# Kernel tuning notes

Hardware: AMD Instinct MI355X
Metric: run time of the kernel (lower is better)

## Reference

```python
import jax, jax.numpy as jnp
import numpy as np

B, N = 16, 48
NODE, EDGE, HID, MSG, LAYERS, TGT = 32, 16, 64, 64, 3, 128
NL = 128  # hidden width of cfg.net_layers / cfg.layers MLPs


def _lin(key, i, o):
    k1, k2 = jax.random.split(key)
    return (jax.random.normal(k1, (i, o), jnp.float32) * 0.05,
            jax.random.normal(k2, (o,), jnp.float32) * 0.05)


def setup_inputs() -> dict:
    key = jax.random.key(0)
    ks = jax.random.split(key, 16)
    g = (jax.random.uniform(ks[0], (B, N, N)) < 0.5).astype(jnp.float32)
    h0 = jax.random.normal(ks[1], (B, N, NODE), jnp.float32)
    e = jax.random.normal(ks[2], (B, N, N, EDGE), jnp.float32)
    msg_w0, msg_b0 = _lin(ks[3], EDGE, NL)
    msg_w1, msg_b1 = _lin(ks[4], NL, NL)
    msg_w2, msg_b2 = _lin(ks[5], NL, MSG * HID)
    gru_wih = jax.random.normal(ks[6], (3 * HID, MSG), jnp.float32) * 0.05
    gru_whh = jax.random.normal(ks[7], (3 * HID, HID), jnp.float32) * 0.05
    gru_bih = jax.random.normal(ks[8], (3 * HID,), jnp.float32) * 0.05
    gru_bhh = jax.random.normal(ks[9], (3 * HID,), jnp.float32) * 0.05
    r0_w0, r0_b0 = _lin(ks[10], 2 * HID, NL)
    r0_w1, r0_b1 = _lin(ks[11], NL, NL)
    r0_w2, r0_b2 = _lin(ks[12], NL, TGT)
    r1_w0, r1_b0 = _lin(ks[13], HID, NL)
    r1_w1, r1_b1 = _lin(ks[14], NL, NL)
    r1_w2, r1_b2 = _lin(ks[15], NL, TGT)
    return dict(g=g, h0=h0, e=e,
                msg_w0=msg_w0, msg_b0=msg_b0, msg_w1=msg_w1, msg_b1=msg_b1,
                msg_w2=msg_w2, msg_b2=msg_b2,
                gru_wih=gru_wih, gru_whh=gru_whh, gru_bih=gru_bih, gru_bhh=gru_bhh,
                r0_w0=r0_w0, r0_b0=r0_b0, r0_w1=r0_w1, r0_b1=r0_b1, r0_w2=r0_w2, r0_b2=r0_b2,
                r1_w0=r1_w0, r1_b0=r1_b0, r1_w1=r1_w1, r1_b1=r1_b1, r1_w2=r1_w2, r1_b2=r1_b2)


def _net(x, w0, b0, w1, b1, w2, b2):
    # Net: relu hidden layers, linear output (matches torch Net with 2 hidden layers)
    x = jax.nn.relu(x @ w0 + b0)
    x = jax.nn.relu(x @ w1 + b1)
    return x @ w2 + b2


def _gru_step(x, h, wih, whh, bih, bhh):
    # torch.nn.GRU single step; gate order r, z, n
    gi = x @ wih.T + bih
    gh = h @ whh.T + bhh
    r = jax.nn.sigmoid(gi[:, :HID] + gh[:, :HID])
    z = jax.nn.sigmoid(gi[:, HID:2 * HID] + gh[:, HID:2 * HID])
    n = jnp.tanh(gi[:, 2 * HID:] + r * gh[:, 2 * HID:])
    return (1.0 - z) * n + z * h


def reference(g, h0, e,
              msg_w0, msg_b0, msg_w1, msg_b1, msg_w2, msg_b2,
              gru_wih, gru_whh, gru_bih, gru_bhh,
              r0_w0, r0_b0, r0_w1, r0_b1, r0_w2, r0_b2,
              r1_w0, r1_b0, r1_w1, r1_b1, r1_w2, r1_b2):
    # pad h0 up to hidden size
    h_first = jnp.concatenate(
        [h0, jnp.zeros((B, N, HID - NODE), h0.dtype)], axis=2)
    node_mask = (jnp.sum(h0, axis=2) > 0).astype(h0.dtype)[..., None]  # [B,N,1]

    # per-edge weight matrices from edge features (same every layer in the
    # original torch code, so compute once): [B*N*N, MSG, HID]
    m_w = _net(e.reshape(-1, EDGE), msg_w0, msg_b0, msg_w1, msg_b1,
               msg_w2, msg_b2).reshape(-1, MSG, HID)

    h_t = h_first
    for _ in range(LAYERS):
        h_feat = h_t.reshape(-1, HID)  # [B*N, HID]
        # faithful to torch: expand on last dim then view(-1, HID),
        # which interleaves the hidden and neighbor axes in memory order
        h_w_rows = jnp.broadcast_to(
            h_feat[:, :, None], (B * N, HID, N)).reshape(-1, HID)
        msg = jnp.einsum('emh,eh->em', m_w, h_w_rows)  # [B*N*N, MSG]
        msg = msg.reshape(B, N, N, MSG)
        agg = jnp.sum(g[..., None] * msg, axis=1)  # masked sum over dim 1 -> [B,N,MSG]
        h_new = _gru_step(agg.reshape(-1, MSG), h_t.reshape(-1, HID),
                          gru_wih, gru_whh, gru_bih, gru_bhh).reshape(B, N, HID)
        h_t = node_mask * h_new

    # readout: Net0(cat[h_0, h_T]) * Net1(h_T), masked by h_0 activity, summed over nodes
    gate_in = jnp.concatenate([h_first, h_t], axis=-1)  # [B,N,2*HID]
    nn_res = (_net(gate_in, r0_w0, r0_b0, r0_w1, r0_b1, r0_w2, r0_b2) *
              _net(h_t, r1_w0, r1_b0, r1_w1, r1_b1, r1_w2, r1_b2))  # [B,N,TGT]
    read_mask = (jnp.sum(h_first, axis=2) > 0).astype(nn_res.dtype)[..., None]
    res = jnp.sum(read_mask * nn_res, axis=1)  # [B,TGT]
    return jax.nn.sigmoid(res)
```

## Files before the change

kernel.cpp:

```cpp
#include <hip/hip_runtime.h>
#include <cmath>

#define B_ 16
#define N_ 48
#define HID_ 64
#define NL_ 128
#define NNODE_ (B_*N_)
#define NEDGE_ (B_*N_*N_)

__device__ __forceinline__ float sigmoidf_(float x){ return 1.0f/(1.0f+expf(-x)); }

__global__ void k_prep(const float* __restrict__ w2, const float* __restrict__ b2,
                       const float* __restrict__ h0,
                       const float* __restrict__ wih, const float* __restrict__ whh,
                       const float* __restrict__ w1,
                       float* __restrict__ A, float* __restrict__ Bm,
                       float* __restrict__ Ab, float* __restrict__ Bb,
                       float* __restrict__ hfirst, float* __restrict__ mask,
                       float* __restrict__ wihT, float* __restrict__ whhT,
                       float* __restrict__ w1T)
{
    int idx = blockIdx.x*256 + threadIdx.x;
    if (idx < 24576) {
        int r = idx >> 13;
        int c = (idx >> 6) & 127;
        int m = idx & 63;
        int t = 48 - 16*r;
        const float* src = w2 + c*4096 + m*64;
        float a = 0.f, b = 0.f;
        for (int k = 0; k < 64; k++){ float v = src[k]; if (k < t) a += v; else b += v; }
        A[idx] = a; Bm[idx] = b;
    } else if (idx < 24768) {
        int i2 = idx - 24576;
        int r = i2 >> 6, m = i2 & 63;
        int t = 48 - 16*r;
        const float* src = b2 + m*64;
        float a = 0.f, b = 0.f;
        for (int k = 0; k < 64; k++){ float v = src[k]; if (k < t) a += v; else b += v; }
        Ab[i2] = a; Bb[i2] = b;
    } else if (idx < 73920) {
        int i3 = idx - 24768;
        int node = i3 >> 6, m = i3 & 63;
        hfirst[i3] = (m < 32) ? h0[node*32 + m] : 0.f;
        if (m == 0) {
            float s = 0.f;
            for (int k = 0; k < 32; k++) s += h0[node*32 + k];
            mask[node] = (s > 0.f) ? 1.f : 0.f;
        }
    } else if (idx < 98496) {
        int i4 = idx - 73920;
        if (i4 < 12288) {
            int k = i4 / 192, col = i4 - k*192;
            wihT[i4] = wih[col*64 + k];
        } else {
            int i5 = i4 - 12288;
            int k = i5 / 192, col = i5 - k*192;
            whhT[i5] = whh[col*64 + k];
        }
    } else if (idx < 114880) {
        int i6 = idx - 98496;
        int o = i6 >> 7, i = i6 & 127;
        w1T[i6] = w1[i*128 + o];
    }
}

__global__ __launch_bounds__(256) void k_mlp(
    const float* __restrict__ ein, const float* __restrict__ w0, const float* __restrict__ b0,
    const float* __restrict__ w1T, const float* __restrict__ b1,
    float* __restrict__ relu2)
{
    __shared__ __align__(16) float x1s[64*132];
    int tid = threadIdx.x;
    int et = tid & 15, ot = tid >> 4;
    int o0 = ot * 8;
    size_t e0 = (size_t)blockIdx.x * 64;

    float acc[4][8];
    {
        float4 ba = *(const float4*)&b0[o0];
        float4 bb = *(const float4*)&b0[o0 + 4];
        #pragma unroll
        for (int q = 0; q < 4; q++){
            acc[q][0]=ba.x; acc[q][1]=ba.y; acc[q][2]=ba.z; acc[q][3]=ba.w;
            acc[q][4]=bb.x; acc[q][5]=bb.y; acc[q][6]=bb.z; acc[q][7]=bb.w;
        }
    }
    #pragma unroll
    for (int i4 = 0; i4 < 4; i4++){
        float4 ev[4];
        #pragma unroll
        for (int q = 0; q < 4; q++)
            ev[q] = *(const float4*)&ein[(e0 + q*16 + et)*16 + i4*4];
        #pragma unroll
        for (int d = 0; d < 4; d++){
            int i = i4*4 + d;
            float4 wa = *(const float4*)&w0[i*128 + o0];
            float4 wb = *(const float4*)&w0[i*128 + o0 + 4];
            #pragma unroll
            for (int q = 0; q < 4; q++){
                float xi = (d==0) ? ev[q].x : (d==1) ? ev[q].y : (d==2) ? ev[q].z : ev[q].w;
                acc[q][0] += xi*wa.x; acc[q][1] += xi*wa.y;
                acc[q][2] += xi*wa.z; acc[q][3] += xi*wa.w;
                acc[q][4] += xi*wb.x; acc[q][5] += xi*wb.y;
                acc[q][6] += xi*wb.z; acc[q][7] += xi*wb.w;
            }
        }
    }
    #pragma unroll
    for (int q = 0; q < 4; q++){
        int e = q*16 + et;
        float4 s0 = make_float4(fmaxf(acc[q][0],0.f), fmaxf(acc[q][1],0.f),
                                fmaxf(acc[q][2],0.f), fmaxf(acc[q][3],0.f));
        float4 s1 = make_float4(fmaxf(acc[q][4],0.f), fmaxf(acc[q][5],0.f),
                                fmaxf(acc[q][6],0.f), fmaxf(acc[q][7],0.f));
        *(float4*)&x1s[e*132 + o0]     = s0;
        *(float4*)&x1s[e*132 + o0 + 4] = s1;
    }
    __syncthreads();

    float a2[4][8];
    {
        float4 ba = *(const float4*)&b1[o0];
        float4 bb = *(const float4*)&b1[o0 + 4];
        #pragma unroll
        for (int q = 0; q < 4; q++){
            a2[q][0]=ba.x; a2[q][1]=ba.y; a2[q][2]=ba.z; a2[q][3]=ba.w;
            a2[q][4]=bb.x; a2[q][5]=bb.y; a2[q][6]=bb.z; a2[q][7]=bb.w;
        }
    }
    for (int i4 = 0; i4 < 32; i4++){
        int i = i4*4;
        float4 wv[8];
        #pragma unroll
        for (int r2 = 0; r2 < 8; r2++)
            wv[r2] = *(const float4*)&w1T[(size_t)(o0 + r2)*128 + i];
        #pragma unroll
        for (int q = 0; q < 4; q++){
            float4 xv = *(const float4*)&x1s[(q*16 + et)*132 + i];
            #pragma unroll
            for (int r2 = 0; r2 < 8; r2++){
                a2[q][r2] += xv.x*wv[r2].x + xv.y*wv[r2].y
                           + xv.z*wv[r2].z + xv.w*wv[r2].w;
            }
        }
    }
    #pragma unroll
    for (int q = 0; q < 4; q++){
        size_t e = e0 + q*16 + et;
        float4 s0 = make_float4(fmaxf(a2[q][0],0.f), fmaxf(a2[q][1],0.f),
                                fmaxf(a2[q][2],0.f), fmaxf(a2[q][3],0.f));
        float4 s1 = make_float4(fmaxf(a2[q][4],0.f), fmaxf(a2[q][5],0.f),
                                fmaxf(a2[q][6],0.f), fmaxf(a2[q][7],0.f));
        *(float4*)&relu2[e*128 + o0]     = s0;
        *(float4*)&relu2[e*128 + o0 + 4] = s1;
    }
}

__global__ __launch_bounds__(256) void k_layer(
    const float* __restrict__ hin, float* __restrict__ hout,
    const float* __restrict__ relu2,
    const float* __restrict__ A, const float* __restrict__ Bm,
    const float* __restrict__ Ab, const float* __restrict__ Bb,
    const float* __restrict__ g, const float* __restrict__ mask,
    const float* __restrict__ wihT, const float* __restrict__ whhT,
    const float* __restrict__ bih, const float* __restrict__ bhh)
{
    int bj = blockIdx.x;
    int b = bj / 48, j = bj - b*48;
    int r = j % 3;
    int p0 = j + j/3;
    int tid = threadIdx.x;
    int base = b*48;
    __shared__ float hs[64], wAs[48], wBs[48];
    __shared__ float pU[2][128], pV[2][128];
    __shared__ float Us[128], Vs[128];
    __shared__ float pC[4][64];
    __shared__ float sAB[2];
    __shared__ float aggs[64], gi[192], gh[192];

    if (tid < 64) hs[tid] = hin[(size_t)bj*64 + tid];
    else if (tid < 112){
        int i = tid - 64;
        int node = base + i;
        float gv = g[(size_t)node*48 + j];
        wAs[i] = gv * hin[(size_t)node*64 + p0];
        wBs[i] = gv * hin[(size_t)node*64 + p0 + 1];
    }
    __syncthreads();
    if (tid < 2){
        const float* src = tid ? wBs : wAs;
        float s = 0.f;
        for (int i = 0; i < 48; i++) s += src[i];
        sAB[tid] = s;
    }
    {
        int c = tid & 127, half = tid >> 7;
        const float* r2b = relu2 + ((size_t)base*48 + j)*128 + c;
        float aU = 0.f, aV = 0.f;
        for (int ii = 0; ii < 24; ii++){
            int i = half*24 + ii;
            float v = r2b[(size_t)i*6144];
            aU += wAs[i]*v; aV += wBs[i]*v;
        }
        pU[half][c] = aU; pV[half][c] = aV;
    }
    __syncthreads();
    if (tid < 128){ Us[tid] = pU[0][tid] + pU[1][tid]; Vs[tid] = pV[0][tid] + pV[1][tid]; }
    __syncthreads();
    {
        int m = tid & 63, cg = tid >> 6;
        const float* Arp = A  + r*8192 + m;
        const float* Brp = Bm + r*8192 + m;
        float a = 0.f;
        for (int cc = 0; cc < 32; cc++){
            int c = cg*32 + cc;
            a += Us[c]*Arp[c*64] + Vs[c]*Brp[c*64];
        }
        pC[cg][m] = a;
    }
    __syncthreads();
    if (tid < 64){
        aggs[tid] = pC[0][tid] + pC[1][tid] + pC[2][tid] + pC[3][tid]
                  + sAB[0]*Ab[r*64 + tid] + sAB[1]*Bb[r*64 + tid];
    }
    __syncthreads();
    if (tid < 192){
        float gacc = bih[tid], hacc = bhh[tid];
        for (int k = 0; k < 64; k++){
            gacc += aggs[k] * wihT[k*192 + tid];
            hacc += hs[k]   * whhT[k*192 + tid];
        }
        gi[tid] = gacc; gh[tid] = hacc;
    }
    __syncthreads();
    if (tid < 64){
        float rr = sigmoidf_(gi[tid] + gh[tid]);
        float zz = sigmoidf_(gi[64+tid] + gh[64+tid]);
        float nn = tanhf(gi[128+tid] + rr*gh[128+tid]);
        float hnew = (1.f - zz)*nn + zz*hs[tid];
        hout[(size_t)bj*64 + tid] = mask[bj] * hnew;
    }
}

__device__ __forceinline__ void rd_layer(
    const float* __restrict__ Xs, const float* __restrict__ W,
    const float* __restrict__ bias, float* __restrict__ Ys,
    int dim, int o, int ng, bool do_relu)
{
    float a0 = bias[o];
    float a1 = a0;
    for (int i = 0; i < dim; i += 4){
        float w0 = W[(size_t)(i+0)*128 + o];
        float w1 = W[(size_t)(i+1)*128 + o];
        float w2 = W[(size_t)(i+2)*128 + o];
        float w3 = W[(size_t)(i+3)*128 + o];
        const float4 x0 = *(const float4*)&Xs[ng*128 + i];
        const float4 x1 = *(const float4*)&Xs[(ng+2)*128 + i];
        a0 += x0.x*w0 + x0.y*w1 + x0.z*w2 + x0.w*w3;
        a1 += x1.x*w0 + x1.y*w1 + x1.z*w2 + x1.w*w3;
    }
    if (do_relu){ a0 = fmaxf(a0, 0.f); a1 = fmaxf(a1, 0.f); }
    Ys[ng*128 + o] = a0;
    Ys[(ng+2)*128 + o] = a1;
}

__global__ __launch_bounds__(256) void k_read(
    const float* __restrict__ hfirst, const float* __restrict__ hT,
    const float* __restrict__ mask,
    const float* __restrict__ w00, const float* __restrict__ b00,
    const float* __restrict__ w01, const float* __restrict__ b01,
    const float* __restrict__ w02, const float* __restrict__ b02,
    const float* __restrict__ w10, const float* __restrict__ b10,
    const float* __restrict__ w11, const float* __restrict__ b11,
    const float* __restrict__ w12, const float* __restrict__ b12,
    float* __restrict__ partial)
{
    __shared__ __align__(16) float xs[4*128];
    __shared__ __align__(16) float ys[4*128];
    __shared__ __align__(16) float zs[4*128];
    __shared__ __align__(16) float os0[4*128];
    __shared__ float mS[4];
    int tid = threadIdx.x;
    int b = blockIdx.x / 12, gg = blockIdx.x - b*12;
    int node0 = b*48 + gg*4;
    int o = tid & 127, ng = tid >> 7;
    if (tid < 4) mS[tid] = mask[node0 + tid];
    for (int i = tid; i < 4*128; i += 256){
        int r = i >> 7, c = i & 127;
        xs[i] = (c < 64) ? hfirst[(size_t)(node0+r)*64 + c]
                         : hT[(size_t)(node0+r)*64 + (c - 64)];
    }
    __syncthreads();
    rd_layer(xs,      w00, b00, ys,  128, o, ng, true);  __syncthreads();
    rd_layer(ys,      w01, b01, zs,  128, o, ng, true);  __syncthreads();
    rd_layer(zs,      w02, b02, os0, 128, o, ng, false); __syncthreads();
    rd_layer(xs + 64, w10, b10, ys,  64,  o, ng, true);  __syncthreads();
    rd_layer(ys,      w11, b11, zs,  128, o, ng, true);  __syncthreads();
    {
        float a0 = b12[o];
        float a1 = a0;
        for (int i = 0; i < 128; i += 4){
            float w0 = w12[(size_t)(i+0)*128 + o];
            float w1 = w12[(size_t)(i+1)*128 + o];
            float w2 = w12[(size_t)(i+2)*128 + o];
            float w3 = w12[(size_t)(i+3)*128 + o];
            const float4 x0 = *(const float4*)&zs[ng*128 + i];
            const float4 x1 = *(const float4*)&zs[(ng+2)*128 + i];
            a0 += x0.x*w0 + x0.y*w1 + x0.z*w2 + x0.w*w3;
            a1 += x1.x*w0 + x1.y*w1 + x1.z*w2 + x1.w*w3;
        }
        float s = mS[ng]   * os0[ng*128 + o]     * a0
                + mS[ng+2] * os0[(ng+2)*128 + o] * a1;
        __syncthreads();
        ys[ng*128 + o] = s;
    }
    __syncthreads();
    if (tid < 128)
        partial[(size_t)blockIdx.x*128 + tid] = ys[tid] + ys[128 + tid];
}

__global__ void k_final(const float* __restrict__ partial, float* __restrict__ out)
{
    int idx = blockIdx.x*256 + threadIdx.x;
    if (idx < B_*128){
        int b = idx >> 7, t = idx & 127;
        float s = 0.f;
        for (int c = 0; c < 12; c++) s += partial[(size_t)(b*12 + c)*128 + t];
        out[idx] = 1.0f / (1.0f + expf(-s));
    }
}

extern "C" void kernel_launch(void* const* d_in, const int* in_sizes, int n_in,
                              void* d_out, int out_size, void* d_ws, size_t ws_size,
                              hipStream_t stream)
{
    (void)in_sizes; (void)n_in; (void)out_size; (void)ws_size;
    const float* g    = (const float*)d_in[0];
    const float* h0   = (const float*)d_in[1];
    const float* e    = (const float*)d_in[2];
    const float* mw0  = (const float*)d_in[3];
    const float* mb0  = (const float*)d_in[4];
    const float* mw1  = (const float*)d_in[5];
    const float* mb1  = (const float*)d_in[6];
    const float* mw2  = (const float*)d_in[7];
    const float* mb2  = (const float*)d_in[8];
    const float* wih  = (const float*)d_in[9];
    const float* whh  = (const float*)d_in[10];
    const float* bih  = (const float*)d_in[11];
    const float* bhh  = (const float*)d_in[12];
    const float* r0w0 = (const float*)d_in[13];
    const float* r0b0 = (const float*)d_in[14];
    const float* r0w1 = (const float*)d_in[15];
    const float* r0b1 = (const float*)d_in[16];
    const float* r0w2 = (const float*)d_in[17];
    const float* r0b2 = (const float*)d_in[18];
    const float* r1w0 = (const float*)d_in[19];
    const float* r1b0 = (const float*)d_in[20];
    const float* r1w1 = (const float*)d_in[21];
    const float* r1b1 = (const float*)d_in[22];
    const float* r1w2 = (const float*)d_in[23];
    const float* r1b2 = (const float*)d_in[24];
    float* out = (float*)d_out;

    float* ws     = (float*)d_ws;
    float* A      = ws;
    float* Bm     = A      + 24576;
    float* Ab     = Bm     + 24576;
    float* Bb     = Ab     + 192;
    float* hfirst = Bb     + 192;
    float* hA     = hfirst + 49152;
    float* hB     = hA     + 49152;
    float* mask   = hB     + 49152;
    float* wihT   = mask   + 768;
    float* whhT   = wihT   + 12288;
    float* w1T    = whhT   + 12288;
    float* part   = w1T    + 16384;
    float* relu2  = part   + 24576;

    k_prep<<<449, 256, 0, stream>>>(mw2, mb2, h0, wih, whh, mw1,
                                    A, Bm, Ab, Bb, hfirst, mask, wihT, whhT, w1T);
    k_mlp<<<576, 256, 0, stream>>>(e, mw0, mb0, w1T, mb1, relu2);
    k_layer<<<768, 256, 0, stream>>>(hfirst, hA, relu2, A, Bm, Ab, Bb, g, mask,
                                     wihT, whhT, bih, bhh);
    k_layer<<<768, 256, 0, stream>>>(hA, hB, relu2, A, Bm, Ab, Bb, g, mask,
                                     wihT, whhT, bih, bhh);
    k_layer<<<768, 256, 0, stream>>>(hB, hA, relu2, A, Bm, Ab, Bb, g, mask,
                                     wihT, whhT, bih, bhh);
    k_read<<<192, 256, 0, stream>>>(hfirst, hA, mask,
                                    r0w0, r0b0, r0w1, r0b1, r0w2, r0b2,
                                    r1w0, r1b0, r1w1, r1b1, r1w2, r1b2, part);
    k_final<<<8, 256, 0, stream>>>(part, out);
}
```

Before: 192.8 us.

## Fuse edge MLP with first GRU layer and last layer with readout

Result: slower. 228.4 us (+18.5%).

```diff
diff --git a/kernel.cpp b/kernel.cpp
--- a/kernel.cpp
+++ b/kernel.cpp
@@ -3,22 +3,16 @@
 
 #define B_ 16
 #define N_ 48
-#define HID_ 64
-#define NL_ 128
-#define NNODE_ (B_*N_)
-#define NEDGE_ (B_*N_*N_)
 
 __device__ __forceinline__ float sigmoidf_(float x){ return 1.0f/(1.0f+expf(-x)); }
 
 __global__ void k_prep(const float* __restrict__ w2, const float* __restrict__ b2,
                        const float* __restrict__ h0,
                        const float* __restrict__ wih, const float* __restrict__ whh,
-                       const float* __restrict__ w1,
                        float* __restrict__ A, float* __restrict__ Bm,
                        float* __restrict__ Ab, float* __restrict__ Bb,
                        float* __restrict__ hfirst, float* __restrict__ mask,
-                       float* __restrict__ wihT, float* __restrict__ whhT,
-                       float* __restrict__ w1T)
+                       float* __restrict__ wihT, float* __restrict__ whhT)
 {
     int idx = blockIdx.x*256 + threadIdx.x;
     if (idx < 24576) {
@@ -57,47 +51,58 @@
             int k = i5 / 192, col = i5 - k*192;
             whhT[i5] = whh[col*64 + k];
         }
-    } else if (idx < 114880) {
-        int i6 = idx - 98496;
-        int o = i6 >> 7, i = i6 & 127;
-        w1T[i6] = w1[i*128 + o];
     }
 }
 
-__global__ __launch_bounds__(256) void k_mlp(
+__global__ __launch_bounds__(256, 3) void k1_mlp_l0(
     const float* __restrict__ ein, const float* __restrict__ w0, const float* __restrict__ b0,
-    const float* __restrict__ w1T, const float* __restrict__ b1,
-    float* __restrict__ relu2)
+    const float* __restrict__ w1, const float* __restrict__ b1,
+    const float* __restrict__ g, const float* __restrict__ h0,
+    const float* __restrict__ mask,
+    const float* __restrict__ A, const float* __restrict__ Bm,
+    const float* __restrict__ Ab, const float* __restrict__ Bb,
+    const float* __restrict__ wihT, const float* __restrict__ whhT,
+    const float* __restrict__ bih, const float* __restrict__ bhh,
+    float* __restrict__ relu2, float* __restrict__ hout)
 {
-    __shared__ __align__(16) float x1s[64*132];
-    int tid = threadIdx.x;
-    int et = tid & 15, ot = tid >> 4;
-    int o0 = ot * 8;
-    size_t e0 = (size_t)blockIdx.x * 64;
-
-    float acc[4][8];
+    __shared__ __align__(16) float smem[12480];
+    float* x1s = smem;
+    float* r2s = smem + 6336;
+    const int tid  = threadIdx.x;
+    const int bj   = blockIdx.x;
+    const int b    = bj / 48, j = bj - b*48;
+    const int base = b*48;
+
+    const int et = tid & 15;
+    const int o0 = (tid >> 4) * 8;
+    size_t eg[3];
+    #pragma unroll
+    for (int q = 0; q < 3; q++)
+        eg[q] = ((size_t)(base + q*16 + et)*48 + j);
+
+    float acc[3][8];
     {
         float4 ba = *(const float4*)&b0[o0];
         float4 bb = *(const float4*)&b0[o0 + 4];
         #pragma unroll
-        for (int q = 0; q < 4; q++){
+        for (int q = 0; q < 3; q++){
             acc[q][0]=ba.x; acc[q][1]=ba.y; acc[q][2]=ba.z; acc[q][3]=ba.w;
             acc[q][4]=bb.x; acc[q][5]=bb.y; acc[q][6]=bb.z; acc[q][7]=bb.w;
         }
     }
     #pragma unroll
     for (int i4 = 0; i4 < 4; i4++){
-        float4 ev[4];
+        float4 ev[3];
         #pragma unroll
-        for (int q = 0; q < 4; q++)
-            ev[q] = *(const float4*)&ein[(e0 + q*16 + et)*16 + i4*4];
+        for (int q = 0; q < 3; q++)
+            ev[q] = *(const float4*)&ein[eg[q]*16 + i4*4];
         #pragma unroll
         for (int d = 0; d < 4; d++){
             int i = i4*4 + d;
             float4 wa = *(const float4*)&w0[i*128 + o0];
             float4 wb = *(const float4*)&w0[i*128 + o0 + 4];
             #pragma unroll
-            for (int q = 0; q < 4; q++){
+            for (int q = 0; q < 3; q++){
                 float xi = (d==0) ? ev[q].x : (d==1) ? ev[q].y : (d==2) ? ev[q].z : ev[q].w;
                 acc[q][0] += xi*wa.x; acc[q][1] += xi*wa.y;
                 acc[q][2] += xi*wa.z; acc[q][3] += xi*wa.w;
@@ -107,52 +112,148 @@
         }
     }
     #pragma unroll
-    for (int q = 0; q < 4; q++){
-        int e = q*16 + et;
-        float4 s0 = make_float4(fmaxf(acc[q][0],0.f), fmaxf(acc[q][1],0.f),
-                                fmaxf(acc[q][2],0.f), fmaxf(acc[q][3],0.f));
-        float4 s1 = make_float4(fmaxf(acc[q][4],0.f), fmaxf(acc[q][5],0.f),
-                                fmaxf(acc[q][6],0.f), fmaxf(acc[q][7],0.f));
-        *(float4*)&x1s[e*132 + o0]     = s0;
-        *(float4*)&x1s[e*132 + o0 + 4] = s1;
-    }
-    __syncthreads();
-
-    float a2[4][8];
+    for (int q = 0; q < 3; q++){
+        int el = q*16 + et;
+        *(float4*)&x1s[el*132 + o0] =
+            make_float4(fmaxf(acc[q][0],0.f), fmaxf(acc[q][1],0.f),
+                        fmaxf(acc[q][2],0.f), fmaxf(acc[q][3],0.f));
+        *(float4*)&x1s[el*132 + o0 + 4] =
+            make_float4(fmaxf(acc[q][4],0.f), fmaxf(acc[q][5],0.f),
+                        fmaxf(acc[q][6],0.f), fmaxf(acc[q][7],0.f));
+    }
+    __syncthreads();
+
+    float a2[3][8];
     {
         float4 ba = *(const float4*)&b1[o0];
         float4 bb = *(const float4*)&b1[o0 + 4];
         #pragma unroll
-        for (int q = 0; q < 4; q++){
+        for (int q = 0; q < 3; q++){
             a2[q][0]=ba.x; a2[q][1]=ba.y; a2[q][2]=ba.z; a2[q][3]=ba.w;
             a2[q][4]=bb.x; a2[q][5]=bb.y; a2[q][6]=bb.z; a2[q][7]=bb.w;
         }
     }
     for (int i4 = 0; i4 < 32; i4++){
         int i = i4*4;
-        float4 wv[8];
+        float4 w0a = *(const float4*)&w1[(size_t)(i+0)*128 + o0];
+        float4 w0b = *(const float4*)&w1[(size_t)(i+0)*128 + o0 + 4];
+        float4 w1a = *(const float4*)&w1[(size_t)(i+1)*128 + o0];
+        float4 w1b = *(const float4*)&w1[(size_t)(i+1)*128 + o0 + 4];
+        float4 w2a = *(const float4*)&w1[(size_t)(i+2)*128 + o0];
+        float4 w2b = *(const float4*)&w1[(size_t)(i+2)*128 + o0 + 4];
+        float4 w3a = *(const float4*)&w1[(size_t)(i+3)*128 + o0];
+        float4 w3b = *(const float4*)&w1[(size_t)(i+3)*128 + o0 + 4];
+        float4 xv[3];
         #pragma unroll
-        for (int r2 = 0; r2 < 8; r2++)
-            wv[r2] = *(const float4*)&w1T[(size_t)(o0 + r2)*128 + i];
+        for (int q = 0; q < 3; q++)
+            xv[q] = *(const float4*)&x1s[(q*16 + et)*132 + i];
         #pragma unroll
-        for (int q = 0; q < 4; q++){
-            float4 xv = *(const float4*)&x1s[(q*16 + et)*132 + i];
-            #pragma unroll
-            for (int r2 = 0; r2 < 8; r2++){
-                a2[q][r2] += xv.x*wv[r2].x + xv.y*wv[r2].y
-                           + xv.z*wv[r2].z + xv.w*wv[r2].w;
-            }
+        for (int q = 0; q < 3; q++){
+            float4 x = xv[q];
+            a2[q][0] += x.x*w0a.x + x.y*w1a.x + x.z*w2a.x + x.w*w3a.x;
+            a2[q][1] += x.x*w0a.y + x.y*w1a.y + x.z*w2a.y + x.w*w3a.y;
+            a2[q][2] += x.x*w0a.z + x.y*w1a.z + x.z*w2a.z + x.w*w3a.z;
+            a2[q][3] += x.x*w0a.w + x.y*w1a.w + x.z*w2a.w + x.w*w3a.w;
+            a2[q][4] += x.x*w0b.x + x.y*w1b.x + x.z*w2b.x + x.w*w3b.x;
+            a2[q][5] += x.x*w0b.y + x.y*w1b.y + x.z*w2b.y + x.w*w3b.y;
+            a2[q][6] += x.x*w0b.z + x.y*w1b.z + x.z*w2b.z + x.w*w3b.z;
+            a2[q][7] += x.x*w0b.w + x.y*w1b.w + x.z*w2b.w + x.w*w3b.w;
         }
     }
     #pragma unroll
-    for (int q = 0; q < 4; q++){
-        size_t e = e0 + q*16 + et;
+    for (int q = 0; q < 3; q++){
+        int el = q*16 + et;
         float4 s0 = make_float4(fmaxf(a2[q][0],0.f), fmaxf(a2[q][1],0.f),
                                 fmaxf(a2[q][2],0.f), fmaxf(a2[q][3],0.f));
         float4 s1 = make_float4(fmaxf(a2[q][4],0.f), fmaxf(a2[q][5],0.f),
                                 fmaxf(a2[q][6],0.f), fmaxf(a2[q][7],0.f));
-        *(float4*)&relu2[e*128 + o0]     = s0;
-        *(float4*)&relu2[e*128 + o0 + 4] = s1;
+        *(float4*)&r2s[el*128 + o0]     = s0;
+        *(float4*)&r2s[el*128 + o0 + 4] = s1;
+        *(float4*)&relu2[eg[q]*128 + o0]     = s0;
+        *(float4*)&relu2[eg[q]*128 + o0 + 4] = s1;
+    }
+    __syncthreads();
+
+    float* hs   = smem;
+    float* wAs  = smem + 64;
+    float* wBs  = smem + 112;
+    float* sAB  = smem + 160;
+    float* pU   = smem + 162;
+    float* pV   = smem + 418;
+    float* Us   = smem + 674;
+    float* Vs   = smem + 802;
+    float* pC   = smem + 930;
+    float* aggs = smem + 1186;
+    float* gi   = smem + 1250;
+    float* gh   = smem + 1442;
+
+    const int r  = j % 3;
+    const int q0 = j + j/3;
+
+    if (tid < 64) hs[tid] = (tid < 32) ? h0[bj*32 + tid] : 0.f;
+    else if (tid < 112){
+        int i = tid - 64;
+        int node = base + i;
+        float gv = g[(size_t)node*48 + j];
+        float ha = (q0   < 32) ? h0[node*32 + q0]     : 0.f;
+        float hb = (q0+1 < 32) ? h0[node*32 + q0 + 1] : 0.f;
+        wAs[i] = gv * ha;
+        wBs[i] = gv * hb;
+    }
+    __syncthreads();
+    if (tid < 2){
+        const float* src = tid ? wBs : wAs;
+        float s = 0.f;
+        for (int i = 0; i < 48; i++) s += src[i];
+        sAB[tid] = s;
+    }
+    {
+        int c = tid & 127, half = tid >> 7;
+        const float* rb = r2s + c;
+        float aU = 0.f, aV = 0.f;
+        for (int ii = 0; ii < 24; ii++){
+            int i = half*24 + ii;
+            float v = rb[i*128];
+            aU += wAs[i]*v; aV += wBs[i]*v;
+        }
+        pU[half*128 + c] = aU; pV[half*128 + c] = aV;
+    }
+    __syncthreads();
+    if (tid < 128){ Us[tid] = pU[tid] + pU[128 + tid]; }
+    else { int c = tid - 128; Vs[c] = pV[c] + pV[128 + c]; }
+    __syncthreads();
+    {
+        int m = tid & 63, cg2 = tid >> 6;
+        const float* Arp = A  + r*8192 + m;
+        const float* Brp = Bm + r*8192 + m;
+        float a = 0.f;
+        for (int cc = 0; cc < 32; cc++){
+            int c = cg2*32 + cc;
+            a += Us[c]*Arp[c*64] + Vs[c]*Brp[c*64];
+        }
+        pC[cg2*64 + m] = a;
+    }
+    __syncthreads();
+    if (tid < 64){
+        aggs[tid] = pC[tid] + pC[64+tid] + pC[128+tid] + pC[192+tid]
+                  + sAB[0]*Ab[r*64 + tid] + sAB[1]*Bb[r*64 + tid];
+    }
+    __syncthreads();
+    if (tid < 192){
+        float gacc = bih[tid], hacc = bhh[tid];
+        for (int k = 0; k < 64; k++){
+            gacc += aggs[k] * wihT[k*192 + tid];
+            hacc += hs[k]   * whhT[k*192 + tid];
+        }
+        gi[tid] = gacc; gh[tid] = hacc;
+    }
+    __syncthreads();
+    if (tid < 64){
+        float rr = sigmoidf_(gi[tid] + gh[tid]);
+        float zz = sigmoidf_(gi[64+tid] + gh[64+tid]);
+        float nn = tanhf(gi[128+tid] + rr*gh[128+tid]);
+        float hnew = (1.f - zz)*nn + zz*hs[tid];
+        hout[(size_t)bj*64 + tid] = mask[bj] * hnew;
     }
 }
 
@@ -242,90 +343,173 @@
     }
 }
 
-__device__ __forceinline__ void rd_layer(
-    const float* __restrict__ Xs, const float* __restrict__ W,
-    const float* __restrict__ bias, float* __restrict__ Ys,
-    int dim, int o, int ng, bool do_relu)
-{
-    float a0 = bias[o];
-    float a1 = a0;
-    for (int i = 0; i < dim; i += 4){
-        float w0 = W[(size_t)(i+0)*128 + o];
-        float w1 = W[(size_t)(i+1)*128 + o];
-        float w2 = W[(size_t)(i+2)*128 + o];
-        float w3 = W[(size_t)(i+3)*128 + o];
-        const float4 x0 = *(const float4*)&Xs[ng*128 + i];
-        const float4 x1 = *(const float4*)&Xs[(ng+2)*128 + i];
-        a0 += x0.x*w0 + x0.y*w1 + x0.z*w2 + x0.w*w3;
-        a1 += x1.x*w0 + x1.y*w1 + x1.z*w2 + x1.w*w3;
-    }
-    if (do_relu){ a0 = fmaxf(a0, 0.f); a1 = fmaxf(a1, 0.f); }
-    Ys[ng*128 + o] = a0;
-    Ys[(ng+2)*128 + o] = a1;
-}
-
-__global__ __launch_bounds__(256) void k_read(
-    const float* __restrict__ hfirst, const float* __restrict__ hT,
-    const float* __restrict__ mask,
+__global__ __launch_bounds__(256) void k3_layer_read(
+    const float* __restrict__ hin,
+    const float* __restrict__ relu2,
+    const float* __restrict__ A, const float* __restrict__ Bm,
+    const float* __restrict__ Ab, const float* __restrict__ Bb,
+    const float* __restrict__ g, const float* __restrict__ mask,
+    const float* __restrict__ wihT, const float* __restrict__ whhT,
+    const float* __restrict__ bih, const float* __restrict__ bhh,
+    const float* __restrict__ hfirst,
     const float* __restrict__ w00, const float* __restrict__ b00,
     const float* __restrict__ w01, const float* __restrict__ b01,
     const float* __restrict__ w02, const float* __restrict__ b02,
     const float* __restrict__ w10, const float* __restrict__ b10,
     const float* __restrict__ w11, const float* __restrict__ b11,
     const float* __restrict__ w12, const float* __restrict__ b12,
-    float* __restrict__ partial)
+    float* __restrict__ part)
 {
-    __shared__ __align__(16) float xs[4*128];
-    __shared__ __align__(16) float ys[4*128];
-    __shared__ __align__(16) float zs[4*128];
-    __shared__ __align__(16) float os0[4*128];
-    __shared__ float mS[4];
+    int bj = blockIdx.x;
+    int b = bj / 48, j = bj - b*48;
+    int r = j % 3;
+    int p0 = j + j/3;
     int tid = threadIdx.x;
-    int b = blockIdx.x / 12, gg = blockIdx.x - b*12;
-    int node0 = b*48 + gg*4;
-    int o = tid & 127, ng = tid >> 7;
-    if (tid < 4) mS[tid] = mask[node0 + tid];
-    for (int i = tid; i < 4*128; i += 256){
-        int r = i >> 7, c = i & 127;
-        xs[i] = (c < 64) ? hfirst[(size_t)(node0+r)*64 + c]
-                         : hT[(size_t)(node0+r)*64 + (c - 64)];
-    }
-    __syncthreads();
-    rd_layer(xs,      w00, b00, ys,  128, o, ng, true);  __syncthreads();
-    rd_layer(ys,      w01, b01, zs,  128, o, ng, true);  __syncthreads();
-    rd_layer(zs,      w02, b02, os0, 128, o, ng, false); __syncthreads();
-    rd_layer(xs + 64, w10, b10, ys,  64,  o, ng, true);  __syncthreads();
-    rd_layer(ys,      w11, b11, zs,  128, o, ng, true);  __syncthreads();
-    {
-        float a0 = b12[o];
-        float a1 = a0;
-        for (int i = 0; i < 128; i += 4){
-            float w0 = w12[(size_t)(i+0)*128 + o];
-            float w1 = w12[(size_t)(i+1)*128 + o];
-            float w2 = w12[(size_t)(i+2)*128 + o];
-            float w3 = w12[(size_t)(i+3)*128 + o];
-            const float4 x0 = *(const float4*)&zs[ng*128 + i];
-            const float4 x1 = *(const float4*)&zs[(ng+2)*128 + i];
-            a0 += x0.x*w0 + x0.y*w1 + x0.z*w2 + x0.w*w3;
-            a1 += x1.x*w0 + x1.y*w1 + x1.z*w2 + x1.w*w3;
-        }
-        float s = mS[ng]   * os0[ng*128 + o]     * a0
-                + mS[ng+2] * os0[(ng+2)*128 + o] * a1;
-        __syncthreads();
-        ys[ng*128 + o] = s;
-    }
-    __syncthreads();
-    if (tid < 128)
-        partial[(size_t)blockIdx.x*128 + tid] = ys[tid] + ys[128 + tid];
+    int base = b*48;
+    __shared__ float hs[64], wAs[48], wBs[48];
+    __shared__ float pU[2][128], pV[2][128];
+    __shared__ float Us[128], Vs[128];
+    __shared__ float pC[4][64];
+    __shared__ float sAB[2];
+    __shared__ float aggs[64], gi[192], gh[192];
+    __shared__ float hfs[64], hTs[64];
+    __shared__ float ps[256], bufA[128], bufB[128], os0[128];
+
+    if (tid < 64) hs[tid] = hin[(size_t)bj*64 + tid];
+    else if (tid < 112){
+        int i = tid - 64;
+        int node = base + i;
+        float gv = g[(size_t)node*48 + j];
+        wAs[i] = gv * hin[(size_t)node*64 + p0];
+        wBs[i] = gv * hin[(size_t)node*64 + p0 + 1];
+    }
+    else if (tid < 176){
+        hfs[tid - 112] = hfirst[(size_t)bj*64 + (tid - 112)];
+    }
+    __syncthreads();
+    if (tid < 2){
+        const float* src = tid ? wBs : wAs;
+        float s = 0.f;
+        for (int i = 0; i < 48; i++) s += src[i];
+        sAB[tid] = s;
+    }
+    {
+        int c = tid & 127, half = tid >> 7;
+        const float* r2b = relu2 + ((size_t)base*48 + j)*128 + c;
+        float aU = 0.f, aV = 0.f;
+        for (int ii = 0; ii < 24; ii++){
+            int i = half*24 + ii;
+            float v = r2b[(size_t)i*6144];
+            aU += wAs[i]*v; aV += wBs[i]*v;
+        }
+        pU[half][c] = aU; pV[half][c] = aV;
+    }
+    __syncthreads();
+    if (tid < 128){ Us[tid] = pU[0][tid] + pU[1][tid]; Vs[tid] = pV[0][tid] + pV[1][tid]; }
+    __syncthreads();
+    {
+        int m = tid & 63, cg = tid >> 6;
+        const float* Arp = A  + r*8192 + m;
+        const float* Brp = Bm + r*8192 + m;
+        float a = 0.f;
+        for (int cc = 0; cc < 32; cc++){
+            int c = cg*32 + cc;
+            a += Us[c]*Arp[c*64] + Vs[c]*Brp[c*64];
+        }
+        pC[cg][m] = a;
+    }
+    __syncthreads();
+    if (tid < 64){
+        aggs[tid] = pC[0][tid] + pC[1][tid] + pC[2][tid] + pC[3][tid]
+                  + sAB[0]*Ab[r*64 + tid] + sAB[1]*Bb[r*64 + tid];
+    }
+    __syncthreads();
+    if (tid < 192){
+        float gacc = bih[tid], hacc = bhh[tid];
+        for (int k = 0; k < 64; k++){
+            gacc += aggs[k] * wihT[k*192 + tid];
+            hacc += hs[k]   * whhT[k*192 + tid];
+        }
+        gi[tid] = gacc; gh[tid] = hacc;
+    }
+    __syncthreads();
+    if (tid < 64){
+        float rr = sigmoidf_(gi[tid] + gh[tid]);
+        float zz = sigmoidf_(gi[64+tid] + gh[64+tid]);
+        float nn = tanhf(gi[128+tid] + rr*gh[128+tid]);
+        float hnew = (1.f - zz)*nn + zz*hs[tid];
+        hTs[tid] = mask[bj] * hnew;
+    }
+    __syncthreads();
+
+    int o = tid & 127, hh = tid >> 7;
+    {
+        float a = 0.f;
+        for (int i = hh*64; i < hh*64 + 64; i++){
+            float x = (i < 64) ? hfs[i] : hTs[i - 64];
+            a += x * w00[(size_t)i*128 + o];
+        }
+        ps[hh*128 + o] = a;
+    }
+    __syncthreads();
+    if (tid < 128) bufA[o] = fmaxf(b00[o] + ps[o] + ps[128 + o], 0.f);
+    __syncthreads();
+    {
+        float a = 0.f;
+        for (int i = hh*64; i < hh*64 + 64; i++)
+            a += bufA[i] * w01[(size_t)i*128 + o];
+        ps[hh*128 + o] = a;
+    }
+    __syncthreads();
+    if (tid < 128) bufB[o] = fmaxf(b01[o] + ps[o] + ps[128 + o], 0.f);
+    __syncthreads();
+    {
+        float a = 0.f;
+        for (int i = hh*64; i < hh*64 + 64; i++)
+            a += bufB[i] * w02[(size_t)i*128 + o];
+        ps[hh*128 + o] = a;
+    }
+    __syncthreads();
+    if (tid < 128) os0[o] = b02[o] + ps[o] + ps[128 + o];
+    __syncthreads();
+    {
+        float a = 0.f;
+        for (int i = hh*32; i < hh*32 + 32; i++)
+            a += hTs[i] * w10[(size_t)i*128 + o];
+        ps[hh*128 + o] = a;
+    }
+    __syncthreads();
+    if (tid < 128) bufA[o] = fmaxf(b10[o] + ps[o] + ps[128 + o], 0.f);
+    __syncthreads();
+    {
+        float a = 0.f;
+        for (int i = hh*64; i < hh*64 + 64; i++)
+            a += bufA[i] * w11[(size_t)i*128 + o];
+        ps[hh*128 + o] = a;
+    }
+    __syncthreads();
+    if (tid < 128) bufB[o] = fmaxf(b11[o] + ps[o] + ps[128 + o], 0.f);
+    __syncthreads();
+    {
+        float a = 0.f;
+        for (int i = hh*64; i < hh*64 + 64; i++)
+            a += bufB[i] * w12[(size_t)i*128 + o];
+        ps[hh*128 + o] = a;
+    }
+    __syncthreads();
+    if (tid < 128){
+        float r1o = b12[o] + ps[o] + ps[128 + o];
+        part[(size_t)bj*128 + o] = mask[bj] * os0[o] * r1o;
+    }
 }
 
-__global__ void k_final(const float* __restrict__ partial, float* __restrict__ out)
+__global__ void k_final(const float* __restrict__ part, float* __restrict__ out)
 {
     int idx = blockIdx.x*256 + threadIdx.x;
     if (idx < B_*128){
         int b = idx >> 7, t = idx & 127;
         float s = 0.f;
-        for (int c = 0; c < 12; c++) s += partial[(size_t)(b*12 + c)*128 + t];
+        for (int n = 0; n < 48; n++) s += part[(size_t)(b*48 + n)*128 + t];
         out[idx] = 1.0f / (1.0f + expf(-s));
     }
 }
@@ -373,21 +557,20 @@
     float* mask   = hB     + 49152;
     float* wihT   = mask   + 768;
     float* whhT   = wihT   + 12288;
-    float* w1T    = whhT   + 12288;
-    float* part   = w1T    + 16384;
-    float* relu2  = part   + 24576;
-
-    k_prep<<<449, 256, 0, stream>>>(mw2, mb2, h0, wih, whh, mw1,
-                                    A, Bm, Ab, Bb, hfirst, mask, wihT, whhT, w1T);
-    k_mlp<<<576, 256, 0, stream>>>(e, mw0, mb0, w1T, mb1, relu2);
-    k_layer<<<768, 256, 0, stream>>>(hfirst, hA, relu2, A, Bm, Ab, Bb, g, mask,
-                                     wihT, whhT, bih, bhh);
+    float* part   = whhT   + 12288;
+    float* relu2  = part   + 98304;
+
+    k_prep<<<385, 256, 0, stream>>>(mw2, mb2, h0, wih, whh,
+                                    A, Bm, Ab, Bb, hfirst, mask, wihT, whhT);
+    k1_mlp_l0<<<768, 256, 0, stream>>>(e, mw0, mb0, mw1, mb1, g, h0, mask,
+                                       A, Bm, Ab, Bb, wihT, whhT, bih, bhh,
+                                       relu2, hA);
     k_layer<<<768, 256, 0, stream>>>(hA, hB, relu2, A, Bm, Ab, Bb, g, mask,
                                      wihT, whhT, bih, bhh);
-    k_layer<<<768, 256, 0, stream>>>(hB, hA, relu2, A, Bm, Ab, Bb, g, mask,
-                                     wihT, whhT, bih, bhh);
-    k_read<<<192, 256, 0, stream>>>(hfirst, hA, mask,
-                                    r0w0, r0b0, r0w1, r0b1, r0w2, r0b2,
-                                    r1w0, r1b0, r1w1, r1b1, r1w2, r1b2, part);
+    k3_layer_read<<<768, 256, 0, stream>>>(hB, relu2, A, Bm, Ab, Bb, g, mask,
+                                           wihT, whhT, bih, bhh, hfirst,
+                                           r0w0, r0b0, r0w1, r0b1, r0w2, r0b2,
+                                           r1w0, r1b0, r1w1, r1b1, r1w2, r1b2,
+                                           part);
     k_final<<<8, 256, 0, stream>>>(part, out);
 }
```

## Fuse edge MLP with first message-passing layer using destination-major edge layout

Applied to the files above, without the earlier changes.

After: 196.2 us. About the same (+1.7%).

```diff
diff --git a/kernel.cpp b/kernel.cpp
--- a/kernel.cpp
+++ b/kernel.cpp
@@ -3,22 +3,18 @@
 
 #define B_ 16
 #define N_ 48
-#define HID_ 64
-#define NL_ 128
-#define NNODE_ (B_*N_)
-#define NEDGE_ (B_*N_*N_)
 
 __device__ __forceinline__ float sigmoidf_(float x){ return 1.0f/(1.0f+expf(-x)); }
 
 __global__ void k_prep(const float* __restrict__ w2, const float* __restrict__ b2,
                        const float* __restrict__ h0,
                        const float* __restrict__ wih, const float* __restrict__ whh,
-                       const float* __restrict__ w1,
+                       const float* __restrict__ e,
                        float* __restrict__ A, float* __restrict__ Bm,
                        float* __restrict__ Ab, float* __restrict__ Bb,
                        float* __restrict__ hfirst, float* __restrict__ mask,
                        float* __restrict__ wihT, float* __restrict__ whhT,
-                       float* __restrict__ w1T)
+                       float* __restrict__ eT)
 {
     int idx = blockIdx.x*256 + threadIdx.x;
     if (idx < 24576) {
@@ -57,47 +53,65 @@
             int k = i5 / 192, col = i5 - k*192;
             whhT[i5] = whh[col*64 + k];
         }
-    } else if (idx < 114880) {
+    } else if (idx < 245952) {
         int i6 = idx - 98496;
-        int o = i6 >> 7, i = i6 & 127;
-        w1T[i6] = w1[i*128 + o];
-    }
-}
-
-__global__ __launch_bounds__(256) void k_mlp(
-    const float* __restrict__ ein, const float* __restrict__ w0, const float* __restrict__ b0,
-    const float* __restrict__ w1T, const float* __restrict__ b1,
-    float* __restrict__ relu2)
-{
-    __shared__ __align__(16) float x1s[64*132];
-    int tid = threadIdx.x;
-    int et = tid & 15, ot = tid >> 4;
-    int o0 = ot * 8;
-    size_t e0 = (size_t)blockIdx.x * 64;
-
-    float acc[4][8];
+        int d4 = i6 & 3;
+        int E  = i6 >> 2;
+        int j  = E % 48;
+        int bi = E / 48;
+        int i  = bi % 48;
+        int b  = bi / 48;
+        float4 v = *(const float4*)&e[(size_t)i6*4];
+        *(float4*)&eT[(((size_t)(b*48 + j)*48 + i)*4 + d4)*4] = v;
+    }
+}
+
+__global__ __launch_bounds__(256, 3) void k1_mlp_l0(
+    const float* __restrict__ eT, const float* __restrict__ w0, const float* __restrict__ b0,
+    const float* __restrict__ w1, const float* __restrict__ b1,
+    const float* __restrict__ g, const float* __restrict__ h0,
+    const float* __restrict__ mask,
+    const float* __restrict__ A, const float* __restrict__ Bm,
+    const float* __restrict__ Ab, const float* __restrict__ Bb,
+    const float* __restrict__ wihT, const float* __restrict__ whhT,
+    const float* __restrict__ bih, const float* __restrict__ bhh,
+    float* __restrict__ relu2T, float* __restrict__ hout)
+{
+    __shared__ __align__(16) float smem[12480];
+    float* x1s = smem;
+    float* r2s = smem + 6336;
+    const int tid  = threadIdx.x;
+    const int bj   = blockIdx.x;
+    const int b    = bj / 48, j = bj - b*48;
+    const int base = b*48;
+
+    const int et = tid & 15;
+    const int o0 = (tid >> 4) * 8;
+    const size_t ebase = (size_t)bj * 48;
+
+    float acc[3][8];
     {
         float4 ba = *(const float4*)&b0[o0];
         float4 bb = *(const float4*)&b0[o0 + 4];
         #pragma unroll
-        for (int q = 0; q < 4; q++){
+        for (int q = 0; q < 3; q++){
             acc[q][0]=ba.x; acc[q][1]=ba.y; acc[q][2]=ba.z; acc[q][3]=ba.w;
             acc[q][4]=bb.x; acc[q][5]=bb.y; acc[q][6]=bb.z; acc[q][7]=bb.w;
         }
     }
     #pragma unroll
     for (int i4 = 0; i4 < 4; i4++){
-        float4 ev[4];
+        float4 ev[3];
         #pragma unroll
-        for (int q = 0; q < 4; q++)
-            ev[q] = *(const float4*)&ein[(e0 + q*16 + et)*16 + i4*4];
+        for (int q = 0; q < 3; q++)
+            ev[q] = *(const float4*)&eT[(ebase + q*16 + et)*16 + i4*4];
         #pragma unroll
         for (int d = 0; d < 4; d++){
             int i = i4*4 + d;
             float4 wa = *(const float4*)&w0[i*128 + o0];
             float4 wb = *(const float4*)&w0[i*128 + o0 + 4];
             #pragma unroll
-            for (int q = 0; q < 4; q++){
+            for (int q = 0; q < 3; q++){
                 float xi = (d==0) ? ev[q].x : (d==1) ? ev[q].y : (d==2) ? ev[q].z : ev[q].w;
                 acc[q][0] += xi*wa.x; acc[q][1] += xi*wa.y;
                 acc[q][2] += xi*wa.z; acc[q][3] += xi*wa.w;
@@ -107,58 +121,154 @@
         }
     }
     #pragma unroll
-    for (int q = 0; q < 4; q++){
-        int e = q*16 + et;
-        float4 s0 = make_float4(fmaxf(acc[q][0],0.f), fmaxf(acc[q][1],0.f),
-                                fmaxf(acc[q][2],0.f), fmaxf(acc[q][3],0.f));
-        float4 s1 = make_float4(fmaxf(acc[q][4],0.f), fmaxf(acc[q][5],0.f),
-                                fmaxf(acc[q][6],0.f), fmaxf(acc[q][7],0.f));
-        *(float4*)&x1s[e*132 + o0]     = s0;
-        *(float4*)&x1s[e*132 + o0 + 4] = s1;
-    }
-    __syncthreads();
-
-    float a2[4][8];
+    for (int q = 0; q < 3; q++){
+        int el = q*16 + et;
+        *(float4*)&x1s[el*132 + o0] =
+            make_float4(fmaxf(acc[q][0],0.f), fmaxf(acc[q][1],0.f),
+                        fmaxf(acc[q][2],0.f), fmaxf(acc[q][3],0.f));
+        *(float4*)&x1s[el*132 + o0 + 4] =
+            make_float4(fmaxf(acc[q][4],0.f), fmaxf(acc[q][5],0.f),
+                        fmaxf(acc[q][6],0.f), fmaxf(acc[q][7],0.f));
+    }
+    __syncthreads();
+
+    float a2[3][8];
     {
         float4 ba = *(const float4*)&b1[o0];
         float4 bb = *(const float4*)&b1[o0 + 4];
         #pragma unroll
-        for (int q = 0; q < 4; q++){
+        for (int q = 0; q < 3; q++){
             a2[q][0]=ba.x; a2[q][1]=ba.y; a2[q][2]=ba.z; a2[q][3]=ba.w;
             a2[q][4]=bb.x; a2[q][5]=bb.y; a2[q][6]=bb.z; a2[q][7]=bb.w;
         }
     }
     for (int i4 = 0; i4 < 32; i4++){
         int i = i4*4;
-        float4 wv[8];
+        float4 w0a = *(const float4*)&w1[(size_t)(i+0)*128 + o0];
+        float4 w0b = *(const float4*)&w1[(size_t)(i+0)*128 + o0 + 4];
+        float4 w1a = *(const float4*)&w1[(size_t)(i+1)*128 + o0];
+        float4 w1b = *(const float4*)&w1[(size_t)(i+1)*128 + o0 + 4];
+        float4 w2a = *(const float4*)&w1[(size_t)(i+2)*128 + o0];
+        float4 w2b = *(const float4*)&w1[(size_t)(i+2)*128 + o0 + 4];
+        float4 w3a = *(const float4*)&w1[(size_t)(i+3)*128 + o0];
+        float4 w3b = *(const float4*)&w1[(size_t)(i+3)*128 + o0 + 4];
+        float4 xv[3];
         #pragma unroll
-        for (int r2 = 0; r2 < 8; r2++)
-            wv[r2] = *(const float4*)&w1T[(size_t)(o0 + r2)*128 + i];
+        for (int q = 0; q < 3; q++)
+            xv[q] = *(const float4*)&x1s[(q*16 + et)*132 + i];
         #pragma unroll
-        for (int q = 0; q < 4; q++){
-            float4 xv = *(const float4*)&x1s[(q*16 + et)*132 + i];
-            #pragma unroll
-            for (int r2 = 0; r2 < 8; r2++){
-                a2[q][r2] += xv.x*wv[r2].x + xv.y*wv[r2].y
-                           + xv.z*wv[r2].z + xv.w*wv[r2].w;
-            }
+        for (int q = 0; q < 3; q++){
+            float4 x = xv[q];
+            a2[q][0] += x.x*w0a.x + x.y*w1a.x + x.z*w2a.x + x.w*w3a.x;
+            a2[q][1] += x.x*w0a.y + x.y*w1a.y + x.z*w2a.y + x.w*w3a.y;
+            a2[q][2] += x.x*w0a.z + x.y*w1a.z + x.z*w2a.z + x.w*w3a.z;
+            a2[q][3] += x.x*w0a.w + x.y*w1a.w + x.z*w2a.w + x.w*w3a.w;
+            a2[q][4] += x.x*w0b.x + x.y*w1b.x + x.z*w2b.x + x.w*w3b.x;
+            a2[q][5] += x.x*w0b.y + x.y*w1b.y + x.z*w2b.y + x.w*w3b.y;
+            a2[q][6] += x.x*w0b.z + x.y*w1b.z + x.z*w2b.z + x.w*w3b.z;
+            a2[q][7] += x.x*w0b.w + x.y*w1b.w + x.z*w2b.w + x.w*w3b.w;
         }
     }
     #pragma unroll
-    for (int q = 0; q < 4; q++){
-        size_t e = e0 + q*16 + et;
+    for (int q = 0; q < 3; q++){
+        int el = q*16 + et;
         float4 s0 = make_float4(fmaxf(a2[q][0],0.f), fmaxf(a2[q][1],0.f),
                                 fmaxf(a2[q][2],0.f), fmaxf(a2[q][3],0.f));
         float4 s1 = make_float4(fmaxf(a2[q][4],0.f), fmaxf(a2[q][5],0.f),
                                 fmaxf(a2[q][6],0.f), fmaxf(a2[q][7],0.f));
-        *(float4*)&relu2[e*128 + o0]     = s0;
-        *(float4*)&relu2[e*128 + o0 + 4] = s1;
+        *(float4*)&r2s[el*128 + o0]     = s0;
+        *(float4*)&r2s[el*128 + o0 + 4] = s1;
+        *(float4*)&relu2T[(ebase + el)*128 + o0]     = s0;
+        *(float4*)&relu2T[(ebase + el)*128 + o0 + 4] = s1;
+    }
+    __syncthreads();
+
+    float* hs   = smem;
+    float* wAs  = smem + 64;
+    float* wBs  = smem + 112;
+    float* sAB  = smem + 160;
+    float* pU   = smem + 162;
+    float* pV   = smem + 418;
+    float* Us   = smem + 674;
+    float* Vs   = smem + 802;
+    float* pC   = smem + 930;
+    float* aggs = smem + 1186;
+    float* gi   = smem + 1250;
+    float* gh   = smem + 1442;
+
+    const int r  = j % 3;
+    const int q0 = j + j/3;
+
+    if (tid < 64) hs[tid] = (tid < 32) ? h0[bj*32 + tid] : 0.f;
+    else if (tid < 112){
+        int i = tid - 64;
+        int node = base + i;
+        float gv = g[(size_t)node*48 + j];
+        float ha = (q0   < 32) ? h0[node*32 + q0]     : 0.f;
+        float hb = (q0+1 < 32) ? h0[node*32 + q0 + 1] : 0.f;
+        wAs[i] = gv * ha;
+        wBs[i] = gv * hb;
+    }
+    __syncthreads();
+    if (tid < 2){
+        const float* src = tid ? wBs : wAs;
+        float s = 0.f;
+        for (int i = 0; i < 48; i++) s += src[i];
+        sAB[tid] = s;
+    }
+    {
+        int c = tid & 127, half = tid >> 7;
+        const float* rb = r2s + c;
+        float aU = 0.f, aV = 0.f;
+        for (int ii = 0; ii < 24; ii++){
+            int i = half*24 + ii;
+            float v = rb[i*128];
+            aU += wAs[i]*v; aV += wBs[i]*v;
+        }
+        pU[half*128 + c] = aU; pV[half*128 + c] = aV;
+    }
+    __syncthreads();
+    if (tid < 128){ Us[tid] = pU[tid] + pU[128 + tid]; }
+    else { int c = tid - 128; Vs[c] = pV[c] + pV[128 + c]; }
+    __syncthreads();
+    {
+        int m = tid & 63, cg2 = tid >> 6;
+        const float* Arp = A  + r*8192 + m;
+        const float* Brp = Bm + r*8192 + m;
+        float a = 0.f;
+        for (int cc = 0; cc < 32; cc++){
+            int c = cg2*32 + cc;
+            a += Us[c]*Arp[c*64] + Vs[c]*Brp[c*64];
+        }
+        pC[cg2*64 + m] = a;
+    }
+    __syncthreads();
+    if (tid < 64){
+        aggs[tid] = pC[tid] + pC[64+tid] + pC[128+tid] + pC[192+tid]
+                  + sAB[0]*Ab[r*64 + tid] + sAB[1]*Bb[r*64 + tid];
+    }
+    __syncthreads();
+    if (tid < 192){
+        float gacc = bih[tid], hacc = bhh[tid];
+        for (int k = 0; k < 64; k++){
+            gacc += aggs[k] * wihT[k*192 + tid];
+            hacc += hs[k]   * whhT[k*192 + tid];
+        }
+        gi[tid] = gacc; gh[tid] = hacc;
+    }
+    __syncthreads();
+    if (tid < 64){
+        float rr = sigmoidf_(gi[tid] + gh[tid]);
+        float zz = sigmoidf_(gi[64+tid] + gh[64+tid]);
+        float nn = tanhf(gi[128+tid] + rr*gh[128+tid]);
+        float hnew = (1.f - zz)*nn + zz*hs[tid];
+        hout[(size_t)bj*64 + tid] = mask[bj] * hnew;
     }
 }
 
 __global__ __launch_bounds__(256) void k_layer(
     const float* __restrict__ hin, float* __restrict__ hout,
-    const float* __restrict__ relu2,
+    const float* __restrict__ relu2T,
     const float* __restrict__ A, const float* __restrict__ Bm,
     const float* __restrict__ Ab, const float* __restrict__ Bb,
     const float* __restrict__ g, const float* __restrict__ mask,
@@ -195,11 +305,11 @@
     }
     {
         int c = tid & 127, half = tid >> 7;
-        const float* r2b = relu2 + ((size_t)base*48 + j)*128 + c;
+        const float* r2b = relu2T + (size_t)bj*6144 + c;
         float aU = 0.f, aV = 0.f;
         for (int ii = 0; ii < 24; ii++){
             int i = half*24 + ii;
-            float v = r2b[(size_t)i*6144];
+            float v = r2b[i*128];
             aU += wAs[i]*v; aV += wBs[i]*v;
         }
         pU[half][c] = aU; pV[half][c] = aV;
@@ -373,18 +483,18 @@
     float* mask   = hB     + 49152;
     float* wihT   = mask   + 768;
     float* whhT   = wihT   + 12288;
-    float* w1T    = whhT   + 12288;
-    float* part   = w1T    + 16384;
-    float* relu2  = part   + 24576;
-
-    k_prep<<<449, 256, 0, stream>>>(mw2, mb2, h0, wih, whh, mw1,
-                                    A, Bm, Ab, Bb, hfirst, mask, wihT, whhT, w1T);
-    k_mlp<<<576, 256, 0, stream>>>(e, mw0, mb0, w1T, mb1, relu2);
-    k_layer<<<768, 256, 0, stream>>>(hfirst, hA, relu2, A, Bm, Ab, Bb, g, mask,
+    float* part   = whhT   + 12288;
+    float* eT     = part   + 24576;
+    float* relu2T = eT     + 589824;
+
+    k_prep<<<961, 256, 0, stream>>>(mw2, mb2, h0, wih, whh, e,
+                                    A, Bm, Ab, Bb, hfirst, mask, wihT, whhT, eT);
+    k1_mlp_l0<<<768, 256, 0, stream>>>(eT, mw0, mb0, mw1, mb1, g, h0, mask,
+                                       A, Bm, Ab, Bb, wihT, whhT, bih, bhh,
+                                       relu2T, hA);
+    k_layer<<<768, 256, 0, stream>>>(hA, hB, relu2T, A, Bm, Ab, Bb, g, mask,
                                      wihT, whhT, bih, bhh);
-    k_layer<<<768, 256, 0, stream>>>(hA, hB, relu2, A, Bm, Ab, Bb, g, mask,
-                                     wihT, whhT, bih, bhh);
-    k_layer<<<768, 256, 0, stream>>>(hB, hA, relu2, A, Bm, Ab, Bb, g, mask,
+    k_layer<<<768, 256, 0, stream>>>(hB, hA, relu2T, A, Bm, Ab, Bb, g, mask,
                                      wihT, whhT, bih, bhh);
     k_read<<<192, 256, 0, stream>>>(hfirst, hA, mask,
                                     r0w0, r0b0, r0w1, r0b1, r0w2, r0b2,
```
